# Performance work log

Hardware: AMD Instinct MI355X
Metric: run time of the kernel (lower is better)

The kernel has to match this reference:

```python
import jax, jax.numpy as jnp
import numpy as np

B, T, D = 2, 2048, 2048
DK = 128           # head_dim (key)
H = D // DK        # 16 heads
NH = 3             # num_householder
DV = 128           # head_dim * expand_v (expand_v=1)
KCONV = 4          # short conv size
SCALE = DK ** -0.5
EPS_L2 = 1e-6
EPS_NORM = 1e-5


def _dwconv_silu(x, w):
    """Causal depthwise conv1d + SiLU. x: [B,T,C], w: [C,K]."""
    C, K = w.shape
    xp = jnp.pad(x, ((0, 0), (K - 1, 0), (0, 0)))
    kern = w.T[:, None, :]  # [K, 1, C] for WIO, groups=C
    y = jax.lax.conv_general_dilated(
        xp, kern, window_strides=(1,), padding='VALID',
        dimension_numbers=('NWC', 'WIO', 'NWC'), feature_group_count=C)
    return jax.nn.silu(y)


def _l2norm(x):
    return x * jax.lax.rsqrt(jnp.sum(x * x, axis=-1, keepdims=True) + EPS_L2)


def setup_inputs() -> dict:
    key = jax.random.key(0)
    ks = jax.random.split(key, 16)
    rn = lambda k, shape, s=0.02: jax.random.normal(k, shape, dtype=jnp.float32) * s
    return {
        'x': jax.random.normal(ks[0], (B, T, D), dtype=jnp.float32),
        'cos': jax.random.normal(ks[1], (T, DK), dtype=jnp.float32),
        'sin': jax.random.normal(ks[2], (T, DK), dtype=jnp.float32),
        'Wq': rn(ks[3], (D, H * DK)),
        'Wk': rn(ks[4], (D, NH * H * DK)),
        'Wv': rn(ks[5], (D, NH * H * DV)),
        'Wb': rn(ks[6], (D, NH * H)),
        'Wa': rn(ks[7], (D, H)),
        'A_log': jnp.log(jax.random.uniform(ks[8], (H,), minval=1.0, maxval=16.0)),
        'dt_bias': rn(ks[9], (H,), 0.5),
        'conv_q': rn(ks[10], (H * DK, KCONV), 0.2),
        'conv_k': rn(ks[11], (NH * H * DK, KCONV), 0.2),
        'conv_v': rn(ks[12], (NH * H * DV, KCONV), 0.2),
        'Wg': rn(ks[13], (D, H * DV)),
        'norm_w': jnp.ones((DV,), dtype=jnp.float32),
        'Wo': rn(ks[14], (H * DV, D)),
    }


def _deltaproduct(x, Wq, Wk, Wv, Wb, Wa, A_log, dt_bias,
                  conv_q, conv_k, conv_v, Wg, norm_w, Wo):
    # projections + causal short conv (SiLU) on q, k, v
    q = _dwconv_silu(x @ Wq, conv_q)                    # [B,T,H*DK]
    k = _dwconv_silu(x @ Wk, conv_k)                    # [B,T,NH*H*DK]
    v = _dwconv_silu(x @ Wv, conv_v)                    # [B,T,NH*H*DV]
    beta = jax.nn.sigmoid(x @ Wb) * 2.0                 # allow_neg_eigval: beta in [0,2]
    g = -jnp.exp(A_log) * jax.nn.softplus(x @ Wa + dt_bias)  # [B,T,H], forget gate (log-decay)

    q = _l2norm(q.reshape(B, T, H, DK)) * SCALE         # [B,T,H,DK]
    k = _l2norm(k.reshape(B, T, NH, H, DK))             # [B,T,NH,H,DK]
    v = v.reshape(B, T, NH, H, DV)
    beta = beta.reshape(B, T, NH, H)

    # gated delta-rule recurrence; NH Householder sub-steps per token,
    # decay applied once per token, query read after all sub-steps.
    def step(S, inp):  # S: [B,H,DK,DV]
        qt, kt, vt, bt, gt = inp   # kt:[B,NH,H,DK] vt:[B,NH,H,DV] bt:[B,NH,H] gt:[B,H]
        S = S * jnp.exp(gt)[:, :, None, None]
        for i in range(NH):
            ki, vi, bi = kt[:, i], vt[:, i], bt[:, i]
            kS = jnp.einsum('bhk,bhkv->bhv', ki, S)
            S = S + jnp.einsum('bhk,bhv->bhkv', ki, bi[..., None] * (vi - kS))
        ot = jnp.einsum('bhk,bhkv->bhv', qt, S)
        return S, ot

    S0 = jnp.zeros((B, H, DK, DV), dtype=x.dtype)
    xs = (jnp.moveaxis(q, 1, 0), jnp.moveaxis(k, 1, 0), jnp.moveaxis(v, 1, 0),
          jnp.moveaxis(beta, 1, 0), jnp.moveaxis(g, 1, 0))
    _, o = jax.lax.scan(step, S0, xs)                   # o: [T,B,H,DV]
    o = jnp.moveaxis(o, 0, 1)                           # [B,T,H,DV]

    # gated RMSNorm over head value dim, then output projection
    gate = (x @ Wg).reshape(B, T, H, DV)
    o = o * jax.lax.rsqrt(jnp.mean(o * o, axis=-1, keepdims=True) + EPS_NORM)
    o = o * norm_w * jax.nn.silu(gate)
    return o.reshape(B, T, H * DV) @ Wo                 # [B,T,D]


def reference(x, cos, sin, Wq, Wk, Wv, Wb, Wa, A_log, dt_bias,
              conv_q, conv_k, conv_v, Wg, norm_w, Wo):
    # cos/sin are accepted but ignored (recurrent layer, no RoPE)
    return _deltaproduct(x, Wq, Wk, Wv, Wb, Wa, A_log, dt_bias,
                         conv_q, conv_k, conv_v, Wg, norm_w, Wo)
```

## Files before the change

kernel.cpp:

```cpp
#include <hip/hip_runtime.h>

#define T_SEQ 2048
#define NB 2
#define HH 16
#define M_ROWS 4096
#define KDIM 2048
#define N1B 14464
#define COL_B 14336
#define COL_A 14384

typedef unsigned short u16;
typedef __attribute__((ext_vector_type(8))) short bf16x8;
typedef __attribute__((ext_vector_type(4))) float f32x4;

__device__ __forceinline__ u16 f2b(float f) {
  union { float f; unsigned u; } a; a.f = f;
  unsigned u = a.u;
  u += 0x7fffu + ((u >> 16) & 1u);
  return (u16)(u >> 16);
}
__device__ __forceinline__ float b2f(u16 s) {
  union { unsigned u; float f; } a; a.u = ((unsigned)s) << 16;
  return a.f;
}
__device__ __forceinline__ float silu_f(float y) {
  return y / (1.f + __expf(-y));
}

__device__ __forceinline__ float rowsum16(float x) {
  int xi;
  xi = __builtin_amdgcn_update_dpp(0, __float_as_int(x), 0x128, 0xf, 0xf, true);
  x += __int_as_float(xi);
  xi = __builtin_amdgcn_update_dpp(0, __float_as_int(x), 0x124, 0xf, 0xf, true);
  x += __int_as_float(xi);
  xi = __builtin_amdgcn_update_dpp(0, __float_as_int(x), 0x122, 0xf, 0xf, true);
  x += __int_as_float(xi);
  xi = __builtin_amdgcn_update_dpp(0, __float_as_int(x), 0x121, 0xf, 0xf, true);
  x += __int_as_float(xi);
  return x;
}

__device__ __forceinline__ void gload_lds16(const u16* g, u16* l) {
  __builtin_amdgcn_global_load_lds(
      (const __attribute__((address_space(1))) unsigned int*)g,
      (__attribute__((address_space(3))) unsigned int*)l, 16, 0, 0);
}

#define UNPK(u, lo, hi) { lo = __uint_as_float((u) << 16); hi = __uint_as_float((u) & 0xffff0000u); }

__device__ __forceinline__ void unpk8(uint4 u, float* f) {
  UNPK(u.x, f[0], f[1]); UNPK(u.y, f[2], f[3]);
  UNPK(u.z, f[4], f[5]); UNPK(u.w, f[6], f[7]);
}

__global__ __launch_bounds__(256) void cvt_x_kernel(const float* __restrict__ x,
                                                    u16* __restrict__ xb) {
  int i = (blockIdx.x * 256 + threadIdx.x) * 4;
  float4 v = *(const float4*)&x[i];
  ushort4 o;
  o.x = f2b(v.x); o.y = f2b(v.y); o.z = f2b(v.z); o.w = f2b(v.w);
  *(ushort4*)&xb[i] = o;
}

__global__ __launch_bounds__(256) void wcat_t_kernel(
    const float* __restrict__ Wq, const float* __restrict__ Wk,
    const float* __restrict__ Wv, const float* __restrict__ Wb,
    const float* __restrict__ Wa, u16* __restrict__ WcatT) {
  __shared__ float tile[32][33];
  int kk0 = blockIdx.x * 32;
  int n0  = blockIdx.y * 32;
  int tx = threadIdx.x, ty = threadIdx.y;
  #pragma unroll
  for (int i = 0; i < 4; i++) {
    int kk = kk0 + ty + i * 8;
    int n = n0 + tx;
    float v;
    if      (n < 2048)  v = Wq[(size_t)kk * 2048 + n];
    else if (n < 8192)  v = Wk[(size_t)kk * 6144 + (n - 2048)];
    else if (n < 14336) v = Wv[(size_t)kk * 6144 + (n - 8192)];
    else if (n < 14384) v = Wb[(size_t)kk * 48 + (n - 14336)];
    else if (n < 14400) v = Wa[(size_t)kk * 16 + (n - 14384)];
    else                v = 0.f;
    tile[ty + i * 8][tx] = v;
  }
  __syncthreads();
  #pragma unroll
  for (int i = 0; i < 4; i++) {
    int n = n0 + ty + i * 8;
    int kk = kk0 + tx;
    WcatT[(size_t)n * 2048 + kk] = f2b(tile[tx][ty + i * 8]);
  }
}

__global__ __launch_bounds__(256) void t2048_kernel(const float* __restrict__ W,
                                                    u16* __restrict__ WT) {
  __shared__ float tile[32][33];
  int kk0 = blockIdx.x * 32;
  int n0  = blockIdx.y * 32;
  int tx = threadIdx.x, ty = threadIdx.y;
  #pragma unroll
  for (int i = 0; i < 4; i++)
    tile[ty + i * 8][tx] = W[(size_t)(kk0 + ty + i * 8) * 2048 + (n0 + tx)];
  __syncthreads();
  #pragma unroll
  for (int i = 0; i < 4; i++)
    WT[(size_t)(n0 + ty + i * 8) * 2048 + (kk0 + tx)] = f2b(tile[tx][ty + i * 8]);
}

template<typename OT>
__global__ __launch_bounds__(256) void gemm_bt_kernel(
    const u16* __restrict__ A, const u16* __restrict__ BT, OT* __restrict__ C,
    int M, int N, int K) {
  __shared__ u16 As[128 * 32];
  __shared__ u16 Bs[128 * 32];
  int tid = threadIdx.x;
  int wave = tid >> 6, lane = tid & 63;
  int wr = (wave >> 1) * 64, wc = (wave & 1) * 64;
  int l15 = lane & 15, l4 = lane >> 4;
  size_t mt = (size_t)blockIdx.y * 128, nt = (size_t)blockIdx.x * 128;
  f32x4 acc[4][4] = {};

  int srow = wave * 32 + (lane >> 2);
  int scol = (lane & 3) * 8;
  const u16* gA0 = &A [(mt + srow) * (size_t)K + scol];
  const u16* gA1 = &A [(mt + srow + 16) * (size_t)K + scol];
  const u16* gB0 = &BT[(nt + srow) * (size_t)K + scol];
  const u16* gB1 = &BT[(nt + srow + 16) * (size_t)K + scol];
  u16* lA0 = &As[wave * 1024];
  u16* lA1 = &As[wave * 1024 + 512];
  u16* lB0 = &Bs[wave * 1024];
  u16* lB1 = &Bs[wave * 1024 + 512];

  for (int k0 = 0; k0 < K; k0 += 32) {
    gload_lds16(gA0 + k0, lA0);
    gload_lds16(gA1 + k0, lA1);
    gload_lds16(gB0 + k0, lB0);
    gload_lds16(gB1 + k0, lB1);
    __syncthreads();
    bf16x8 af[4], bvf[4];
    #pragma unroll
    for (int m = 0; m < 4; m++) af[m] = *(const bf16x8*)&As[(wr + m * 16 + l15) * 32 + l4 * 8];
    #pragma unroll
    for (int n = 0; n < 4; n++) bvf[n] = *(const bf16x8*)&Bs[(wc + n * 16 + l15) * 32 + l4 * 8];
    #pragma unroll
    for (int m = 0; m < 4; m++)
      #pragma unroll
      for (int n = 0; n < 4; n++)
        acc[m][n] = __builtin_amdgcn_mfma_f32_16x16x32_bf16(af[m], bvf[n], acc[m][n], 0, 0, 0);
    __syncthreads();
  }
  #pragma unroll
  for (int m = 0; m < 4; m++)
    #pragma unroll
    for (int n = 0; n < 4; n++)
      #pragma unroll
      for (int r = 0; r < 4; r++) {
        size_t row = mt + wr + m * 16 + l4 * 4 + r;
        size_t col = nt + wc + n * 16 + l15;
        if constexpr (sizeof(OT) == 2) C[row * (size_t)N + col] = f2b(acc[m][n][r]);
        else                           C[row * (size_t)N + col] = acc[m][n][r];
      }
}

__global__ __launch_bounds__(256) void conv_act_kernel(
    const u16* __restrict__ P,
    const float* __restrict__ conv_q, const float* __restrict__ conv_k,
    const float* __restrict__ conv_v, const float* __restrict__ A_log,
    const float* __restrict__ dt_bias,
    u16* __restrict__ qs, u16* __restrict__ ks, u16* __restrict__ vs,
    float* __restrict__ betag) {
  __shared__ float buf[14336];
  __shared__ float partial[256];
  __shared__ float scl[64];
  int row = blockIdx.x;
  int t = row & (T_SEQ - 1);
  int tid = threadIdx.x;
  const size_t prow = (size_t)row * N1B;

  for (int cb = tid; cb < 1792; cb += 256) {
    int ch = cb * 8;
    float x0[8], x1[8], x2[8], x3[8];
    #pragma unroll
    for (int j = 0; j < 8; j++) { x1[j] = 0.f; x2[j] = 0.f; x3[j] = 0.f; }
    unpk8(*(const uint4*)&P[prow + ch], x0);
    if (t >= 1) unpk8(*(const uint4*)&P[prow - N1B + ch], x1);
    if (t >= 2) unpk8(*(const uint4*)&P[prow - 2 * N1B + ch], x2);
    if (t >= 3) unpk8(*(const uint4*)&P[prow - 3 * N1B + ch], x3);
    const float* w8;
    if (ch < 2048)      w8 = &conv_q[ch * 4];
    else if (ch < 8192) w8 = &conv_k[(ch - 2048) * 4];
    else                w8 = &conv_v[(ch - 8192) * 4];
    float r[8];
    #pragma unroll
    for (int j = 0; j < 8; j++) {
      float4 w = *(const float4*)&w8[j * 4];
      float acc = w.w * x0[j] + w.z * x1[j] + w.y * x2[j] + w.x * x3[j];
      r[j] = silu_f(acc);
    }
    *(float4*)&buf[ch]     = make_float4(r[0], r[1], r[2], r[3]);
    *(float4*)&buf[ch + 4] = make_float4(r[4], r[5], r[6], r[7]);
  }
  __syncthreads();
  {
    int vec = tid >> 2, part = tid & 3;
    int base = (vec < 16) ? vec * 128 : 2048 + (vec - 16) * 128;
    float s = 0.f;
    #pragma unroll
    for (int i = 0; i < 8; i++) {
      float4 v4 = *(const float4*)&buf[base + part * 32 + i * 4];
      s += v4.x * v4.x + v4.y * v4.y + v4.z * v4.z + v4.w * v4.w;
    }
    partial[tid] = s;
  }
  __syncthreads();
  if (tid < 64) {
    float tot = partial[tid * 4] + partial[tid * 4 + 1] + partial[tid * 4 + 2] + partial[tid * 4 + 3];
    float sc = rsqrtf(tot + 1e-6f);
    if (tid < 16) sc *= 0.08838834764831845f;
    scl[tid] = sc;
  }
  __syncthreads();
  for (int cb = tid; cb < 1792; cb += 256) {
    int ch = cb * 8;
    float4 y0 = *(const float4*)&buf[ch];
    float4 y1 = *(const float4*)&buf[ch + 4];
    float sc; u16* dst;
    if (ch < 2048)      { sc = scl[ch >> 7];              dst = &qs[(size_t)row * 2048 + ch]; }
    else if (ch < 8192) { int r = ch - 2048; sc = scl[16 + (r >> 7)]; dst = &ks[(size_t)row * 6144 + r]; }
    else                { int r = ch - 8192; sc = 1.f;    dst = &vs[(size_t)row * 6144 + r]; }
    ushort4 s0, s1;
    s0.x = f2b(y0.x * sc); s0.y = f2b(y0.y * sc); s0.z = f2b(y0.z * sc); s0.w = f2b(y0.w * sc);
    s1.x = f2b(y1.x * sc); s1.y = f2b(y1.y * sc); s1.z = f2b(y1.z * sc); s1.w = f2b(y1.w * sc);
    *(ushort4*)dst = s0;
    *(ushort4*)(dst + 4) = s1;
  }
  if (tid < 16) {
    int h = tid;
    float b0 = b2f(P[prow + COL_B + h]);
    float b1 = b2f(P[prow + COL_B + 16 + h]);
    float b2 = b2f(P[prow + COL_B + 32 + h]);
    float pa = b2f(P[prow + COL_A + h]) + dt_bias[h];
    float sp = (pa > 20.f) ? pa : log1pf(__expf(pa));
    float4 bg;
    bg.x = 2.f / (1.f + __expf(-b0));
    bg.y = 2.f / (1.f + __expf(-b1));
    bg.z = 2.f / (1.f + __expf(-b2));
    bg.w = __expf(-__expf(A_log[h]) * sp);
    *(float4*)&betag[((size_t)row * 16 + h) * 4] = bg;
  }
}

struct Step {
  uint4 qa;
  uint4 ka, kb, kc;
  float va, vb, vc;
  float4 bg;
};

#define SUBSTEP(KV, VV, BBv) { \
  float k0_, k1_, k2_, k3_, k4_, k5_, k6_, k7_; \
  UNPK((KV).x, k0_, k1_); UNPK((KV).y, k2_, k3_); \
  UNPK((KV).z, k4_, k5_); UNPK((KV).w, k6_, k7_); \
  float p = ((k0_ * S0 + k1_ * S1) + (k2_ * S2 + k3_ * S3)) \
          + ((k4_ * S4 + k5_ * S5) + (k6_ * S6 + k7_ * S7)); \
  p = rowsum16(p); \
  float uu = (BBv) * ((VV) - p); \
  S0 += k0_ * uu; S1 += k1_ * uu; S2 += k2_ * uu; S3 += k3_ * uu; \
  S4 += k4_ * uu; S5 += k5_ * uu; S6 += k6_ * uu; S7 += k7_ * uu; }

__global__ __launch_bounds__(256) void scan_kernel(
    const u16* __restrict__ qs, const u16* __restrict__ ks,
    const u16* __restrict__ vs, const float* __restrict__ betag,
    float* __restrict__ os) {
  int blk = blockIdx.x;
  int vchunk = blk & 7, bh = blk >> 3;
  int h = bh & 15, b = bh >> 4;
  int tid = threadIdx.x;
  int c = tid >> 4, kl = tid & 15;
  int v = vchunk * 16 + c;
  float S0 = 0, S1 = 0, S2 = 0, S3 = 0, S4 = 0, S5 = 0, S6 = 0, S7 = 0;

  const size_t qbase = ((size_t)b * T_SEQ) * 2048 + h * 128 + kl * 8;
  const size_t kbase = ((size_t)b * T_SEQ) * 6144 + h * 128 + kl * 8;
  const size_t vbase = ((size_t)b * T_SEQ) * 6144 + h * 128 + v;
  const size_t obase = ((size_t)b * T_SEQ) * 2048 + h * 128 + v;
  const size_t bgbase = ((size_t)b * T_SEQ * 16 + h) * 4;

  auto loadStep = [&](Step& s, int t) {
    s.qa = *(const uint4*)&qs[qbase + (size_t)t * 2048];
    size_t rk = kbase + (size_t)t * 6144;
    s.ka = *(const uint4*)&ks[rk];
    s.kb = *(const uint4*)&ks[rk + 2048];
    s.kc = *(const uint4*)&ks[rk + 4096];
    size_t rv = vbase + (size_t)t * 6144;
    s.va = b2f(vs[rv]); s.vb = b2f(vs[rv + 2048]); s.vc = b2f(vs[rv + 4096]);
    s.bg = *(const float4*)&betag[bgbase + (size_t)t * 64];
  };
  auto compute = [&](const Step& s, int t) {
    float e = s.bg.w;
    S0 *= e; S1 *= e; S2 *= e; S3 *= e; S4 *= e; S5 *= e; S6 *= e; S7 *= e;
    SUBSTEP(s.ka, s.va, s.bg.x);
    SUBSTEP(s.kb, s.vb, s.bg.y);
    SUBSTEP(s.kc, s.vc, s.bg.z);
    float q0_, q1_, q2_, q3_, q4_, q5_, q6_, q7_;
    UNPK(s.qa.x, q0_, q1_); UNPK(s.qa.y, q2_, q3_);
    UNPK(s.qa.z, q4_, q5_); UNPK(s.qa.w, q6_, q7_);
    float p = ((q0_ * S0 + q1_ * S1) + (q2_ * S2 + q3_ * S3))
            + ((q4_ * S4 + q5_ * S5) + (q6_ * S6 + q7_ * S7));
    p = rowsum16(p);
    if (kl == 0) os[obase + (size_t)t * 2048] = p;
  };

  Step sA, sB, sC, sD;
  loadStep(sA, 0); loadStep(sB, 1);
  for (int t = 0; t < T_SEQ; t += 4) {
    loadStep(sC, t + 2); loadStep(sD, t + 3);
    compute(sA, t); compute(sB, t + 1);
    int t4 = (t + 4 < T_SEQ) ? t + 4 : T_SEQ - 1;
    int t5 = (t + 5 < T_SEQ) ? t + 5 : T_SEQ - 1;
    loadStep(sA, t4); loadStep(sB, t5);
    compute(sC, t + 2); compute(sD, t + 3);
  }
}

__global__ __launch_bounds__(256) void norm_gate_kernel(
    const float* __restrict__ os, const u16* __restrict__ gb,
    const float* __restrict__ norm_w, u16* __restrict__ ob) {
  int row = blockIdx.x, tid = threadIdx.x;
  int hh = tid >> 4, l = tid & 15;
  size_t obase = (size_t)row * 2048 + hh * 128 + l * 8;
  float4 o0 = *(const float4*)&os[obase];
  float4 o1 = *(const float4*)&os[obase + 4];
  float ss = o0.x * o0.x + o0.y * o0.y + o0.z * o0.z + o0.w * o0.w
           + o1.x * o1.x + o1.y * o1.y + o1.z * o1.z + o1.w * o1.w;
  ss = rowsum16(ss);
  float sc = rsqrtf(ss * (1.f / 128.f) + 1e-5f);
  uint4 gv = *(const uint4*)&gb[obase];
  float4 w0 = *(const float4*)&norm_w[l * 8];
  float4 w1 = *(const float4*)&norm_w[l * 8 + 4];
  float gv0 = silu_f(b2f((u16)(gv.x & 0xffffu))), gv1 = silu_f(b2f((u16)(gv.x >> 16)));
  float gv2 = silu_f(b2f((u16)(gv.y & 0xffffu))), gv3 = silu_f(b2f((u16)(gv.y >> 16)));
  float gv4 = silu_f(b2f((u16)(gv.z & 0xffffu))), gv5 = silu_f(b2f((u16)(gv.z >> 16)));
  float gv6 = silu_f(b2f((u16)(gv.w & 0xffffu))), gv7 = silu_f(b2f((u16)(gv.w >> 16)));
  ushort4 r0, r1;
  r0.x = f2b(o0.x * sc * w0.x * gv0);
  r0.y = f2b(o0.y * sc * w0.y * gv1);
  r0.z = f2b(o0.z * sc * w0.z * gv2);
  r0.w = f2b(o0.w * sc * w0.w * gv3);
  r1.x = f2b(o1.x * sc * w1.x * gv4);
  r1.y = f2b(o1.y * sc * w1.y * gv5);
  r1.z = f2b(o1.z * sc * w1.z * gv6);
  r1.w = f2b(o1.w * sc * w1.w * gv7);
  *(ushort4*)&ob[obase] = r0;
  *(ushort4*)&ob[obase + 4] = r1;
}

extern "C" void kernel_launch(void* const* d_in, const int* in_sizes, int n_in,
                              void* d_out, int out_size, void* d_ws, size_t ws_size,
                              hipStream_t stream) {
  (void)in_sizes; (void)n_in; (void)out_size; (void)ws_size;
  const float* x       = (const float*)d_in[0];
  const float* Wq      = (const float*)d_in[3];
  const float* Wk      = (const float*)d_in[4];
  const float* Wv      = (const float*)d_in[5];
  const float* Wb      = (const float*)d_in[6];
  const float* Wa      = (const float*)d_in[7];
  const float* A_log   = (const float*)d_in[8];
  const float* dt_bias = (const float*)d_in[9];
  const float* conv_q  = (const float*)d_in[10];
  const float* conv_k  = (const float*)d_in[11];
  const float* conv_v  = (const float*)d_in[12];
  const float* Wg      = (const float*)d_in[13];
  const float* norm_w  = (const float*)d_in[14];
  const float* Wo      = (const float*)d_in[15];

  char* ws = (char*)d_ws;
  constexpr size_t SZ_XB    = (size_t)M_ROWS * KDIM * 2;
  constexpr size_t SZ_WCAT  = (size_t)N1B * KDIM * 2;
  constexpr size_t SZ_P1    = (size_t)M_ROWS * N1B * 2;
  constexpr size_t SZ_QS    = (size_t)M_ROWS * 2048 * 2;
  constexpr size_t SZ_VS    = (size_t)M_ROWS * 6144 * 2;

  u16*   xb    = (u16*)(ws);
  u16*   WcatT = (u16*)(ws + SZ_XB);
  u16*   P1    = (u16*)(ws + SZ_XB + SZ_WCAT);
  u16*   qs    = (u16*)(ws + SZ_XB + SZ_WCAT + SZ_P1);
  u16*   vs    = (u16*)(ws + SZ_XB + SZ_WCAT + SZ_P1 + SZ_QS);
  float* betag = (float*)(ws + SZ_XB + SZ_WCAT + SZ_P1 + SZ_QS + SZ_VS);
  u16*   ks  = WcatT;
  char*  rp  = (char*)P1;
  float* os  = (float*)(rp);
  u16*   WgT = (u16*)(rp + 33554432);
  u16*   gb  = (u16*)(rp + 33554432 + 8388608);
  u16*   ob  = (u16*)(rp + 33554432 + 8388608 + 16777216);
  u16*   WoT = (u16*)(rp + 33554432 + 8388608 + 16777216 + 16777216);

  cvt_x_kernel<<<(M_ROWS * KDIM) / 1024, 256, 0, stream>>>(x, xb);
  wcat_t_kernel<<<dim3(64, N1B / 32), dim3(32, 8), 0, stream>>>(Wq, Wk, Wv, Wb, Wa, WcatT);
  gemm_bt_kernel<u16><<<dim3(N1B / 128, M_ROWS / 128), 256, 0, stream>>>(xb, WcatT, P1,
                                                                         M_ROWS, N1B, KDIM);
  conv_act_kernel<<<M_ROWS, 256, 0, stream>>>(P1, conv_q, conv_k, conv_v, A_log, dt_bias,
                                              qs, ks, vs, betag);
  scan_kernel<<<NB * HH * 8, 256, 0, stream>>>(qs, ks, vs, betag, os);
  t2048_kernel<<<dim3(64, 64), dim3(32, 8), 0, stream>>>(Wg, WgT);
  gemm_bt_kernel<u16><<<dim3(2048 / 128, M_ROWS / 128), 256, 0, stream>>>(xb, WgT, gb,
                                                                          M_ROWS, 2048, KDIM);
  norm_gate_kernel<<<M_ROWS, 256, 0, stream>>>(os, gb, norm_w, ob);
  t2048_kernel<<<dim3(64, 64), dim3(32, 8), 0, stream>>>(Wo, WoT);
  gemm_bt_kernel<float><<<dim3(2048 / 128, M_ROWS / 128), 256, 0, stream>>>(ob, WoT, (float*)d_out,
                                                                            M_ROWS, 2048, KDIM);
}
```

Baseline: 1.423 ms.

## Chunk the delta-product scan with precomputed per-chunk WY/triangular-solve coefficients

Adds a k1 kernel that, for each 4-timestep chunk, computes the key/query Gram matrix with MFMA, combines the decay factors and solves the unit-lower-triangular system for the 12 Householder substeps. The results go to a chunk buffer. The scan kernel then advances the state once per chunk: all 12 k·S and 4 q·S dot products are taken in parallel against the chunk-start state and corrected through the precomputed coefficients. This removes the serial dependency of the 12 rowsum reductions per chunk. The cost is an extra kernel launch, an extra workspace buffer, more registers for prefetched chunks and LDS syncs, plus possible numeric differences from the reordered computation.

After: 1.837 ms. 1.29x slower.

```diff
diff --git a/kernel.cpp b/kernel.cpp
--- a/kernel.cpp
+++ b/kernel.cpp
@@ -8,6 +8,8 @@
 #define N1B 14464
 #define COL_B 14336
 #define COL_A 14384
+#define NCH 512
+#define CBSZ 240
 
 typedef unsigned short u16;
 typedef __attribute__((ext_vector_type(8))) short bf16x8;
@@ -250,27 +252,147 @@
   }
 }
 
-struct Step {
-  uint4 qa;
-  uint4 ka, kb, kc;
-  float va, vb, vc;
-  float4 bg;
-};
-
-#define SUBSTEP(KV, VV, BBv) { \
-  float k0_, k1_, k2_, k3_, k4_, k5_, k6_, k7_; \
-  UNPK((KV).x, k0_, k1_); UNPK((KV).y, k2_, k3_); \
-  UNPK((KV).z, k4_, k5_); UNPK((KV).w, k6_, k7_); \
-  float p = ((k0_ * S0 + k1_ * S1) + (k2_ * S2 + k3_ * S3)) \
-          + ((k4_ * S4 + k5_ * S5) + (k6_ * S6 + k7_ * S7)); \
-  p = rowsum16(p); \
-  float uu = (BBv) * ((VV) - p); \
-  S0 += k0_ * uu; S1 += k1_ * uu; S2 += k2_ * uu; S3 += k3_ * uu; \
-  S4 += k4_ * uu; S5 += k5_ * uu; S6 += k6_ * uu; S7 += k7_ * uu; }
+__global__ __launch_bounds__(64) void k1_kernel(
+    const u16* __restrict__ qs, const u16* __restrict__ ks,
+    const float* __restrict__ betag, float* __restrict__ chunkbuf) {
+  int blk = blockIdx.x;
+  int cc = blk & (NCH - 1), bh = blk >> 9;
+  int h = bh & 15, b = bh >> 4;
+  int lane = threadIdx.x;
+  int t0 = cc * 4;
+  size_t bT = (size_t)b * T_SEQ;
+  __shared__ u16 m16[16 * 128];
+  __shared__ float gram[16][16];
+  __shared__ float sc[40];
+  __shared__ float Ml[12][12];
+
+  #pragma unroll
+  for (int it = 0; it < 4; it++) {
+    int seg = it * 64 + lane;
+    int row = seg >> 4, part = seg & 15;
+    const u16* src;
+    if (row < 12) src = &ks[(bT + t0 + row / 3) * 6144 + (row % 3) * 2048 + h * 128 + part * 8];
+    else          src = &qs[(bT + t0 + (row - 12)) * 2048 + h * 128 + part * 8];
+    *(uint4*)&m16[row * 128 + part * 8] = *(const uint4*)src;
+  }
+  if (lane < 4) {
+    float4 bg = *(const float4*)&betag[((bT + t0 + lane) * 16 + h) * 4];
+    sc[lane * 3 + 0] = bg.x; sc[lane * 3 + 1] = bg.y; sc[lane * 3 + 2] = bg.z;
+    sc[12 + lane] = bg.w;
+  }
+  __syncthreads();
+
+  int l15 = lane & 15, l4 = lane >> 4;
+  f32x4 acc = {};
+  #pragma unroll
+  for (int kk = 0; kk < 4; kk++) {
+    bf16x8 f = *(const bf16x8*)&m16[l15 * 128 + kk * 32 + l4 * 8];
+    acc = __builtin_amdgcn_mfma_f32_16x16x32_bf16(f, f, acc, 0, 0, 0);
+  }
+  #pragma unroll
+  for (int r = 0; r < 4; r++) gram[l4 * 4 + r][l15] = acc[r];
+  if (lane == 0) {
+    float e0 = sc[12], e1 = sc[13], e2 = sc[14], e3 = sc[15];
+    sc[16 + 0] = 1.f;  sc[16 + 1] = e1; sc[16 + 2] = e1 * e2; sc[16 + 3] = e1 * e2 * e3;
+    sc[20 + 1] = 1.f;  sc[20 + 2] = e2; sc[20 + 3] = e2 * e3;
+    sc[24 + 2] = 1.f;  sc[24 + 3] = e3;
+    sc[28 + 3] = 1.f;
+    sc[32] = e0; sc[33] = e0 * e1; sc[34] = e0 * e1 * e2; sc[35] = e0 * e1 * e2 * e3;
+  }
+  __syncthreads();
+
+  if (lane < 12) {
+    int j = lane;
+    for (int i = 0; i < j; i++)
+      Ml[j][i] = sc[j] * sc[16 + (i / 3) * 4 + (j / 3)] * gram[j][i];
+  }
+  __syncthreads();
+
+  float* out = &chunkbuf[((size_t)bh * NCH + cc) * CBSZ];
+  if (lane < 12) {
+    float x[12];
+    #pragma unroll
+    for (int j = 0; j < 12; j++) {
+      float s = (j == lane) ? 1.f : 0.f;
+      #pragma unroll
+      for (int p = 0; p < j; p++) s -= Ml[j][p] * x[p];
+      x[j] = (j < lane) ? 0.f : s;
+    }
+    #pragma unroll
+    for (int j = 0; j < 12; j++) out[j * 12 + lane] = x[j];
+    int sj = lane / 3;
+    #pragma unroll
+    for (int t = 0; t < 4; t++)
+      out[144 + t * 12 + lane] = (sj <= t) ? sc[16 + sj * 4 + t] * gram[12 + t][lane] : 0.f;
+    out[192 + lane] = sc[lane] * sc[32 + sj];
+    out[204 + lane] = sc[16 + sj * 4 + 3];
+    out[216 + lane] = sc[lane];
+  }
+  if (lane < 4) out[228 + lane] = sc[32 + lane];
+  if (lane >= 32 && lane < 40) out[200 + lane] = 0.f;
+}
+
+#define LOADKQV(KR, QR, VF, CC) { \
+  int t0_ = (CC) * 4; \
+  _Pragma("unroll") \
+  for (int j = 0; j < 12; j++) \
+    KR[j] = *(const uint4*)&ks[kbase + (size_t)(t0_ + j / 3) * 6144 + (j % 3) * 2048]; \
+  _Pragma("unroll") \
+  for (int t = 0; t < 4; t++) \
+    QR[t] = *(const uint4*)&qs[qbase + (size_t)(t0_ + t) * 2048]; \
+  _Pragma("unroll") \
+  for (int j = 0; j < 12; j++) \
+    VF[j] = b2f(vs[vbase + (size_t)(t0_ + j / 3) * 6144 + (j % 3) * 2048]); }
+
+#define COMPUTE_CHUNK(KR, QR, VF, CBP, CC) { \
+  const float* cbp_ = (CBP); \
+  float p_[12], pi_[4]; \
+  _Pragma("unroll") \
+  for (int j = 0; j < 12; j++) { \
+    float k0_,k1_,k2_,k3_,k4_,k5_,k6_,k7_; \
+    UNPK(KR[j].x,k0_,k1_); UNPK(KR[j].y,k2_,k3_); \
+    UNPK(KR[j].z,k4_,k5_); UNPK(KR[j].w,k6_,k7_); \
+    float d_ = ((k0_*S0+k1_*S1)+(k2_*S2+k3_*S3))+((k4_*S4+k5_*S5)+(k6_*S6+k7_*S7)); \
+    p_[j] = rowsum16(d_); } \
+  _Pragma("unroll") \
+  for (int t = 0; t < 4; t++) { \
+    float q0_,q1_,q2_,q3_,q4_,q5_,q6_,q7_; \
+    UNPK(QR[t].x,q0_,q1_); UNPK(QR[t].y,q2_,q3_); \
+    UNPK(QR[t].z,q4_,q5_); UNPK(QR[t].w,q6_,q7_); \
+    float d_ = ((q0_*S0+q1_*S1)+(q2_*S2+q3_*S3))+((q4_*S4+q5_*S5)+(q6_*S6+q7_*S7)); \
+    pi_[t] = rowsum16(d_); } \
+  float bv_[12]; \
+  _Pragma("unroll") \
+  for (int j = 0; j < 12; j++) \
+    bv_[j] = cbp_[216 + j] * VF[j] - cbp_[192 + j] * p_[j]; \
+  float u_[12]; \
+  _Pragma("unroll") \
+  for (int j = 0; j < 12; j++) { \
+    float s_ = bv_[j]; \
+    _Pragma("unroll") \
+    for (int i = 0; i < j; i++) s_ += cbp_[j * 12 + i] * bv_[i]; \
+    u_[j] = s_; } \
+  float g3_ = cbp_[231]; \
+  S0 *= g3_; S1 *= g3_; S2 *= g3_; S3 *= g3_; \
+  S4 *= g3_; S5 *= g3_; S6 *= g3_; S7 *= g3_; \
+  _Pragma("unroll") \
+  for (int j = 0; j < 12; j++) { \
+    float w_ = cbp_[204 + j] * u_[j]; \
+    float k0_,k1_,k2_,k3_,k4_,k5_,k6_,k7_; \
+    UNPK(KR[j].x,k0_,k1_); UNPK(KR[j].y,k2_,k3_); \
+    UNPK(KR[j].z,k4_,k5_); UNPK(KR[j].w,k6_,k7_); \
+    S0 += k0_*w_; S1 += k1_*w_; S2 += k2_*w_; S3 += k3_*w_; \
+    S4 += k4_*w_; S5 += k5_*w_; S6 += k6_*w_; S7 += k7_*w_; } \
+  _Pragma("unroll") \
+  for (int t = 0; t < 4; t++) { \
+    float o_ = cbp_[228 + t] * pi_[t]; \
+    _Pragma("unroll") \
+    for (int j = 0; j < 12; j++) o_ += cbp_[144 + t * 12 + j] * u_[j]; \
+    if (kl == 0) os[obase + (size_t)((CC) * 4 + t) * 2048] = o_; } }
 
 __global__ __launch_bounds__(256) void scan_kernel(
     const u16* __restrict__ qs, const u16* __restrict__ ks,
-    const u16* __restrict__ vs, const float* __restrict__ betag,
+    const u16* __restrict__ vs, const float* __restrict__ chunkbuf,
     float* __restrict__ os) {
   int blk = blockIdx.x;
   int vchunk = blk & 7, bh = blk >> 3;
@@ -280,46 +402,35 @@
   int v = vchunk * 16 + c;
   float S0 = 0, S1 = 0, S2 = 0, S3 = 0, S4 = 0, S5 = 0, S6 = 0, S7 = 0;
 
-  const size_t qbase = ((size_t)b * T_SEQ) * 2048 + h * 128 + kl * 8;
-  const size_t kbase = ((size_t)b * T_SEQ) * 6144 + h * 128 + kl * 8;
-  const size_t vbase = ((size_t)b * T_SEQ) * 6144 + h * 128 + v;
-  const size_t obase = ((size_t)b * T_SEQ) * 2048 + h * 128 + v;
-  const size_t bgbase = ((size_t)b * T_SEQ * 16 + h) * 4;
-
-  auto loadStep = [&](Step& s, int t) {
-    s.qa = *(const uint4*)&qs[qbase + (size_t)t * 2048];
-    size_t rk = kbase + (size_t)t * 6144;
-    s.ka = *(const uint4*)&ks[rk];
-    s.kb = *(const uint4*)&ks[rk + 2048];
-    s.kc = *(const uint4*)&ks[rk + 4096];
-    size_t rv = vbase + (size_t)t * 6144;
-    s.va = b2f(vs[rv]); s.vb = b2f(vs[rv + 2048]); s.vc = b2f(vs[rv + 4096]);
-    s.bg = *(const float4*)&betag[bgbase + (size_t)t * 64];
-  };
-  auto compute = [&](const Step& s, int t) {
-    float e = s.bg.w;
-    S0 *= e; S1 *= e; S2 *= e; S3 *= e; S4 *= e; S5 *= e; S6 *= e; S7 *= e;
-    SUBSTEP(s.ka, s.va, s.bg.x);
-    SUBSTEP(s.kb, s.vb, s.bg.y);
-    SUBSTEP(s.kc, s.vc, s.bg.z);
-    float q0_, q1_, q2_, q3_, q4_, q5_, q6_, q7_;
-    UNPK(s.qa.x, q0_, q1_); UNPK(s.qa.y, q2_, q3_);
-    UNPK(s.qa.z, q4_, q5_); UNPK(s.qa.w, q6_, q7_);
-    float p = ((q0_ * S0 + q1_ * S1) + (q2_ * S2 + q3_ * S3))
-            + ((q4_ * S4 + q5_ * S5) + (q6_ * S6 + q7_ * S7));
-    p = rowsum16(p);
-    if (kl == 0) os[obase + (size_t)t * 2048] = p;
-  };
-
-  Step sA, sB, sC, sD;
-  loadStep(sA, 0); loadStep(sB, 1);
-  for (int t = 0; t < T_SEQ; t += 4) {
-    loadStep(sC, t + 2); loadStep(sD, t + 3);
-    compute(sA, t); compute(sB, t + 1);
-    int t4 = (t + 4 < T_SEQ) ? t + 4 : T_SEQ - 1;
-    int t5 = (t + 5 < T_SEQ) ? t + 5 : T_SEQ - 1;
-    loadStep(sA, t4); loadStep(sB, t5);
-    compute(sC, t + 2); compute(sD, t + 3);
+  size_t bT = (size_t)b * T_SEQ;
+  const size_t qbase = bT * 2048 + h * 128 + kl * 8;
+  const size_t kbase = bT * 6144 + h * 128 + kl * 8;
+  const size_t vbase = bT * 6144 + h * 128 + v;
+  const size_t obase = bT * 2048 + h * 128 + v;
+  const float* cbg = &chunkbuf[(size_t)bh * NCH * CBSZ];
+
+  __shared__ float cbl[2][CBSZ];
+  uint4 krA[12], krB[12], qrA[4], qrB[4];
+  float vfA[12], vfB[12];
+
+  if (tid < CBSZ) cbl[0][tid] = cbg[tid];
+  LOADKQV(krA, qrA, vfA, 0);
+  __syncthreads();
+
+  for (int cc = 0; cc < NCH; cc += 2) {
+    float tmp1 = 0.f, tmp2 = 0.f;
+    if (tid < CBSZ) tmp1 = cbg[(size_t)(cc + 1) * CBSZ + tid];
+    LOADKQV(krB, qrB, vfB, cc + 1);
+    COMPUTE_CHUNK(krA, qrA, vfA, cbl[0], cc);
+    if (tid < CBSZ) cbl[1][tid] = tmp1;
+    __syncthreads();
+
+    int nn = (cc + 2 < NCH) ? cc + 2 : NCH - 1;
+    if (tid < CBSZ) tmp2 = cbg[(size_t)nn * CBSZ + tid];
+    LOADKQV(krA, qrA, vfA, nn);
+    COMPUTE_CHUNK(krB, qrB, vfB, cbl[1], cc + 1);
+    if (tid < CBSZ) cbl[0][tid] = tmp2;
+    __syncthreads();
   }
 }
 
@@ -394,6 +505,7 @@
   u16*   gb  = (u16*)(rp + 33554432 + 8388608);
   u16*   ob  = (u16*)(rp + 33554432 + 8388608 + 16777216);
   u16*   WoT = (u16*)(rp + 33554432 + 8388608 + 16777216 + 16777216);
+  float* chunkbuf = (float*)(rp + (size_t)80 * 1024 * 1024);
 
   cvt_x_kernel<<<(M_ROWS * KDIM) / 1024, 256, 0, stream>>>(x, xb);
   wcat_t_kernel<<<dim3(64, N1B / 32), dim3(32, 8), 0, stream>>>(Wq, Wk, Wv, Wb, Wa, WcatT);
@@ -401,7 +513,8 @@
                                                                          M_ROWS, N1B, KDIM);
   conv_act_kernel<<<M_ROWS, 256, 0, stream>>>(P1, conv_q, conv_k, conv_v, A_log, dt_bias,
                                               qs, ks, vs, betag);
-  scan_kernel<<<NB * HH * 8, 256, 0, stream>>>(qs, ks, vs, betag, os);
+  k1_kernel<<<NB * HH * NCH, 64, 0, stream>>>(qs, ks, betag, chunkbuf);
+  scan_kernel<<<NB * HH * 8, 256, 0, stream>>>(qs, ks, vs, chunkbuf, os);
   t2048_kernel<<<dim3(64, 64), dim3(32, 8), 0, stream>>>(Wg, WgT);
   gemm_bt_kernel<u16><<<dim3(2048 / 128, M_ROWS / 128), 256, 0, stream>>>(xb, WgT, gb,
                                                                           M_ROWS, 2048, KDIM);
```

## Overlap scan with gate GEMM and Wo transpose in one launch

Applied to the files above, without the earlier changes.

Merges the recurrent scan, the gate projection GEMM (x@Wg) and the Wo transpose into a single launch, with the block index deciding which role each block takes. The scan uses only 256 blocks and runs long sequentially, so the independent GEMM and transpose blocks can fill the idle compute units alongside it instead of running afterwards. The cost is that the kernel's register and LDS footprint is the union of all three bodies, which may lower occupancy of the scan or GEMM blocks. It also relies on the scan blocks being scheduled first so they are not delayed behind the other work.

New measurement: 1.490 ms. 1.05x slower.

```diff
diff --git a/kernel.cpp b/kernel.cpp
--- a/kernel.cpp
+++ b/kernel.cpp
@@ -92,12 +92,10 @@
   }
 }
 
-__global__ __launch_bounds__(256) void t2048_kernel(const float* __restrict__ W,
-                                                    u16* __restrict__ WT) {
+__device__ __forceinline__ void t2048_body(const float* __restrict__ W,
+                                           u16* __restrict__ WT,
+                                           int kk0, int n0, int tx, int ty) {
   __shared__ float tile[32][33];
-  int kk0 = blockIdx.x * 32;
-  int n0  = blockIdx.y * 32;
-  int tx = threadIdx.x, ty = threadIdx.y;
   #pragma unroll
   for (int i = 0; i < 4; i++)
     tile[ty + i * 8][tx] = W[(size_t)(kk0 + ty + i * 8) * 2048 + (n0 + tx)];
@@ -107,17 +105,21 @@
     WT[(size_t)(n0 + ty + i * 8) * 2048 + (kk0 + tx)] = f2b(tile[tx][ty + i * 8]);
 }
 
+__global__ __launch_bounds__(256) void t2048_kernel(const float* __restrict__ W,
+                                                    u16* __restrict__ WT) {
+  t2048_body(W, WT, blockIdx.x * 32, blockIdx.y * 32, threadIdx.x, threadIdx.y);
+}
+
 template<typename OT>
-__global__ __launch_bounds__(256) void gemm_bt_kernel(
+__device__ __forceinline__ void gemm_body(
     const u16* __restrict__ A, const u16* __restrict__ BT, OT* __restrict__ C,
-    int M, int N, int K) {
+    int M, int N, int K, int bx, int by, int tid) {
   __shared__ u16 As[128 * 32];
   __shared__ u16 Bs[128 * 32];
-  int tid = threadIdx.x;
   int wave = tid >> 6, lane = tid & 63;
   int wr = (wave >> 1) * 64, wc = (wave & 1) * 64;
   int l15 = lane & 15, l4 = lane >> 4;
-  size_t mt = (size_t)blockIdx.y * 128, nt = (size_t)blockIdx.x * 128;
+  size_t mt = (size_t)by * 128, nt = (size_t)bx * 128;
   f32x4 acc[4][4] = {};
 
   int srow = wave * 32 + (lane >> 2);
@@ -160,6 +162,13 @@
         if constexpr (sizeof(OT) == 2) C[row * (size_t)N + col] = f2b(acc[m][n][r]);
         else                           C[row * (size_t)N + col] = acc[m][n][r];
       }
+}
+
+template<typename OT>
+__global__ __launch_bounds__(256) void gemm_bt_kernel(
+    const u16* __restrict__ A, const u16* __restrict__ BT, OT* __restrict__ C,
+    int M, int N, int K) {
+  gemm_body<OT>(A, BT, C, M, N, K, blockIdx.x, blockIdx.y, threadIdx.x);
 }
 
 __global__ __launch_bounds__(256) void conv_act_kernel(
@@ -268,14 +277,27 @@
   S0 += k0_ * uu; S1 += k1_ * uu; S2 += k2_ * uu; S3 += k3_ * uu; \
   S4 += k4_ * uu; S5 += k5_ * uu; S6 += k6_ * uu; S7 += k7_ * uu; }
 
-__global__ __launch_bounds__(256) void scan_kernel(
+__global__ __launch_bounds__(256) void scan_fuse_kernel(
     const u16* __restrict__ qs, const u16* __restrict__ ks,
     const u16* __restrict__ vs, const float* __restrict__ betag,
-    float* __restrict__ os) {
-  int blk = blockIdx.x;
+    float* __restrict__ os,
+    const u16* __restrict__ gA, const u16* __restrict__ gBT, u16* __restrict__ gC,
+    const float* __restrict__ Wo, u16* __restrict__ WoT) {
+  int bid = blockIdx.x;
+  int tid = threadIdx.x;
+  if (bid >= 768) {
+    int flat = bid - 768;
+    t2048_body(Wo, WoT, (flat & 63) * 32, (flat >> 6) * 32, tid & 31, tid >> 5);
+    return;
+  }
+  if (bid >= 256) {
+    int flat = bid - 256;
+    gemm_body<u16>(gA, gBT, gC, M_ROWS, 2048, KDIM, flat & 15, flat >> 4, tid);
+    return;
+  }
+  int blk = bid;
   int vchunk = blk & 7, bh = blk >> 3;
   int h = bh & 15, b = bh >> 4;
-  int tid = threadIdx.x;
   int c = tid >> 4, kl = tid & 15;
   int v = vchunk * 16 + c;
   float S0 = 0, S1 = 0, S2 = 0, S3 = 0, S4 = 0, S5 = 0, S6 = 0, S7 = 0;
@@ -401,12 +423,10 @@
                                                                          M_ROWS, N1B, KDIM);
   conv_act_kernel<<<M_ROWS, 256, 0, stream>>>(P1, conv_q, conv_k, conv_v, A_log, dt_bias,
                                               qs, ks, vs, betag);
-  scan_kernel<<<NB * HH * 8, 256, 0, stream>>>(qs, ks, vs, betag, os);
   t2048_kernel<<<dim3(64, 64), dim3(32, 8), 0, stream>>>(Wg, WgT);
-  gemm_bt_kernel<u16><<<dim3(2048 / 128, M_ROWS / 128), 256, 0, stream>>>(xb, WgT, gb,
-                                                                          M_ROWS, 2048, KDIM);
+  scan_fuse_kernel<<<256 + 512 + 4096, 256, 0, stream>>>(qs, ks, vs, betag, os,
+                                                         xb, WgT, gb, Wo, WoT);
   norm_gate_kernel<<<M_ROWS, 256, 0, stream>>>(os, gb, norm_w, ob);
-  t2048_kernel<<<dim3(64, 64), dim3(32, 8), 0, stream>>>(Wo, WoT);
   gemm_bt_kernel<float><<<dim3(2048 / 128, M_ROWS / 128), 256, 0, stream>>>(ob, WoT, (float*)d_out,
                                                                             M_ROWS, 2048, KDIM);
 }
```
